# Kernel optimization log

Hardware: AMD Instinct MI355X
Metric: run time of the kernel (lower is better)

Reference implementation:

```python
import jax, jax.numpy as jnp
import numpy as np

B, N, E, L = 64, 50000, 1600000, 20
BN_EPS = 1e-5


def setup_inputs() -> dict:
    key = jax.random.key(0)
    ks = jax.random.split(key, 8)
    x = jax.random.normal(ks[0], (B, N), dtype=jnp.float32)
    edge_index = jax.random.randint(ks[1], (2, E), 0, N, dtype=jnp.int32)
    alpha = jax.random.normal(ks[2], (E,), dtype=jnp.float32)
    bias = jax.random.normal(ks[3], (E,), dtype=jnp.float32)
    # LazyLinear(num_labels) on [B, N] features
    W = jax.random.normal(ks[4], (L, N), dtype=jnp.float32) / np.sqrt(N)
    b_lin = jax.random.normal(ks[5], (L,), dtype=jnp.float32) * 0.01
    # LazyBatchNorm1d affine params over N features
    gamma = jnp.ones((N,), dtype=jnp.float32)
    beta = jnp.zeros((N,), dtype=jnp.float32)
    return {"x": x, "edge_index": edge_index, "alpha": alpha, "bias": bias,
            "W": W, "b_lin": b_lin, "gamma": gamma, "beta": beta}


def reference(x, edge_index, alpha, bias, W, b_lin, gamma, beta):
    src, dst = edge_index[0], edge_index[1]
    # gather per-edge source features and apply per-edge affine: [B, E]
    x_e = alpha * x[:, src] + bias
    # scatter-mean into destination nodes: [B, N]
    sums = jnp.zeros((x.shape[0], N), dtype=x.dtype).at[:, dst].add(x_e)
    counts = jnp.zeros((N,), dtype=x.dtype).at[dst].add(1.0)
    x_hat = sums / jnp.maximum(counts, 1.0)
    out = jnp.tanh(x_hat)
    # linear head: [B, L]
    pred = x_hat @ W.T + b_lin
    # BatchNorm1d (training mode: batch stats, biased variance)
    mu = jnp.mean(out, axis=0)
    var = jnp.var(out, axis=0)
    bn = (out - mu) / jnp.sqrt(var + BN_EPS) * gamma + beta
    return (pred, bn)
```

## Files before the change

kernel.cpp:

```cpp
#include <hip/hip_runtime.h>
#include <math.h>

#define NB 64
#define NL 20
#define BN_EPS 1e-5f

#define BIN_W 16
#define NBIN 3125
#define BIN_CAP 640
#define CHUNK 4096

#define NSB 49
#define NSBP 64
#define CAP1 36864
#define NSLICE 9

#define RB 128
#define BPR 25

__device__ __forceinline__ unsigned short f2bf(float f) {
    unsigned u = __float_as_uint(f);
    unsigned r = u + 0x7fff + ((u >> 16) & 1);
    return (unsigned short)(r >> 16);
}

__global__ __launch_bounds__(1024) void stage_kernel(
    const float* __restrict__ x, unsigned short* __restrict__ xTb,
    const int* __restrict__ src, const int* __restrict__ dst,
    const float* __restrict__ alpha, const float* __restrict__ bias,
    int* __restrict__ cnt1, uint2* __restrict__ buf1, int E, int Nn, int nA) {
    __shared__ unsigned hist[NSBP];
    __shared__ unsigned gbase[NSBP];
    __shared__ float tile[64][65];

    int tid = threadIdx.x;

    if ((int)blockIdx.x < nA) {
        int e0 = blockIdx.x * CHUNK;
        if (tid < NSBP) hist[tid] = 0;
        __syncthreads();

        uint2 pay[4];
        unsigned rk[4];
        int sb[4];
        #pragma unroll
        for (int k = 0; k < 4; ++k) {
            int e = e0 + k * 1024 + tid;
            sb[k] = -1;
            if (e < E) {
                int d = dst[e];
                int b = d >> 4;
                int dl = d & 15;
                pay[k].x = (unsigned)src[e] | ((unsigned)f2bf(alpha[e]) << 16);
                pay[k].y = (unsigned)f2bf(bias[e]) | ((unsigned)dl << 16) |
                           ((unsigned)b << 20);
                sb[k] = d >> 10;
                rk[k] = atomicAdd(&hist[sb[k]], 1u);
            }
        }
        __syncthreads();

        if (tid < NSBP) {
            unsigned v = hist[tid];
            if (v > 0) gbase[tid] = (unsigned)atomicAdd(&cnt1[tid], (int)v);
        }
        __syncthreads();

        #pragma unroll
        for (int k = 0; k < 4; ++k) {
            if (sb[k] >= 0) {
                unsigned di = gbase[sb[k]] + rk[k];
                if (di < CAP1)
                    buf1[(size_t)sb[k] * CAP1 + di] = pay[k];
            }
        }
    } else {
        int n0 = ((int)blockIdx.x - nA) * 64;
        int ln = tid & 63;
        int wv = tid >> 6;
        for (int r = wv; r < 64; r += 16) {
            int col = n0 + ln;
            tile[r][ln] = (col < Nn) ? x[r * Nn + col] : 0.f;
        }
        __syncthreads();
        for (int r = wv; r < 64; r += 16) {
            int node = n0 + r;
            if (node < Nn) xTb[(size_t)node * 64 + ln] = f2bf(tile[ln][r]);
        }
    }
}

__global__ __launch_bounds__(1024) void binB_kernel(
    const int* __restrict__ cnt1, const uint2* __restrict__ buf1,
    int* __restrict__ cursor, uint2* __restrict__ paybins) {
    __shared__ unsigned hist[64];
    __shared__ unsigned gbase[64];

    int tid = threadIdx.x;
    int sb = blockIdx.x / NSLICE;
    int slice = blockIdx.x % NSLICE;

    int lim = cnt1[sb];
    if (lim > CAP1) lim = CAP1;
    int cc = lim - slice * 4096;
    if (cc < 0) cc = 0;
    if (cc > 4096) cc = 4096;
    const uint2* pb = buf1 + (size_t)sb * CAP1 + (size_t)slice * 4096;

    if (tid < 64) hist[tid] = 0;
    __syncthreads();

    uint2 pay[4];
    unsigned rk[4];
    int lb[4];
    #pragma unroll
    for (int k = 0; k < 4; ++k) {
        int i = k * 1024 + tid;
        lb[k] = -1;
        if (i < cc) {
            pay[k] = pb[i];
            lb[k] = (int)((pay[k].y >> 20) & 63u);
            rk[k] = atomicAdd(&hist[lb[k]], 1u);
        }
    }
    __syncthreads();

    if (tid < 64) {
        unsigned v = hist[tid];
        if (v > 0)
            gbase[tid] = (unsigned)atomicAdd(&cursor[sb * 64 + tid], (int)v);
    }
    __syncthreads();

    #pragma unroll
    for (int k = 0; k < 4; ++k) {
        if (lb[k] >= 0) {
            int bin = sb * 64 + lb[k];
            unsigned di = gbase[lb[k]] + rk[k];
            if (di < BIN_CAP)
                paybins[(size_t)bin * BIN_CAP + di] = pay[k];
        }
    }
}

__global__ __launch_bounds__(256) void pull_fin5_kernel(
    const int* __restrict__ cursor, const uint2* __restrict__ paybins,
    const unsigned short* __restrict__ xTb, const float* __restrict__ W,
    const float* __restrict__ gamma, const float* __restrict__ beta,
    float* __restrict__ pred_part, float* __restrict__ bn, int Nn) {
    __shared__ __align__(16) char smem[8448];
    uint2* ed = (uint2*)smem;
    float (*xh)[66] = (float (*)[66])smem;
    float (*th)[66] = (float (*)[66])(smem + 4224);

    __shared__ float wl[NL][16];
    __shared__ unsigned h2[16], b2[16], c2[16];
    __shared__ float mu_s[16], a_s[16], be_s[16];

    const unsigned* xTbu = (const unsigned*)xTb;

    int bin = blockIdx.x;
    int tid = threadIdx.x;
    int ln = tid & 63;
    int w = tid >> 6;
    int n0 = bin * 16;
    int pair = ln >> 5;
    int h = ln & 31;

    int cnt = cursor[bin];
    if (cnt > BIN_CAP) cnt = BIN_CAP;
    const uint2* pb = paybins + (size_t)bin * BIN_CAP;

    for (int i = tid; i < NL * 16; i += 256) {
        int l = i >> 4, j = i & 15;
        wl[l][j] = W[l * Nn + n0 + j];
    }
    if (tid < 16) { h2[tid] = 0; c2[tid] = 0; }
    __syncthreads();

    uint2 pA = {0, 0}, pB = {0, 0}, pC = {0, 0};
    {
        if (tid < cnt) { pA = pb[tid]; atomicAdd(&h2[(pA.y >> 16) & 15], 1u); }
        if (tid + 256 < cnt) { pB = pb[tid + 256]; atomicAdd(&h2[(pB.y >> 16) & 15], 1u); }
        if (tid + 512 < cnt) { pC = pb[tid + 512]; atomicAdd(&h2[(pC.y >> 16) & 15], 1u); }
    }
    __syncthreads();

    if (tid < 16) {
        unsigned v = h2[tid];
        unsigned incl = v;
        #pragma unroll
        for (int off = 1; off < 16; off <<= 1) {
            unsigned t = __shfl_up(incl, off, 64);
            if (tid >= off) incl += t;
        }
        b2[tid] = incl - v;
    }
    __syncthreads();

    {
        if (tid < cnt) {
            unsigned dl = (pA.y >> 16) & 15;
            ed[b2[dl] + atomicAdd(&c2[dl], 1u)] = pA;
        }
        if (tid + 256 < cnt) {
            unsigned dl = (pB.y >> 16) & 15;
            ed[b2[dl] + atomicAdd(&c2[dl], 1u)] = pB;
        }
        if (tid + 512 < cnt) {
            unsigned dl = (pC.y >> 16) & 15;
            ed[b2[dl] + atomicAdd(&c2[dl], 1u)] = pC;
        }
    }
    __syncthreads();

    float xv_reg[4], tv_reg[4];
    #pragma unroll
    for (int k = 0; k < 4; ++k) {
        int dl = w * 4 + k;
        int node = n0 + dl;
        int n = (int)h2[dl];
        unsigned bs = b2[dl];
        float accL0 = 0.f, accH0 = 0.f, accL1 = 0.f, accH1 = 0.f;
        float bs0 = 0.f, bs1 = 0.f;
        int j = 0;
        for (; j + 3 < n; j += 4) {
            uint2 e0 = ed[bs + j + pair];
            uint2 e1 = ed[bs + j + 2 + pair];
            unsigned v0 = xTbu[(size_t)(e0.x & 0xffffu) * 32 + h];
            unsigned v1 = xTbu[(size_t)(e1.x & 0xffffu) * 32 + h];
            float al0 = __uint_as_float(e0.x & 0xffff0000u);
            float al1 = __uint_as_float(e1.x & 0xffff0000u);
            bs0 += __uint_as_float((e0.y & 0xffffu) << 16);
            bs1 += __uint_as_float((e1.y & 0xffffu) << 16);
            accL0 = fmaf(al0, __uint_as_float(v0 << 16), accL0);
            accH0 = fmaf(al0, __uint_as_float(v0 & 0xffff0000u), accH0);
            accL1 = fmaf(al1, __uint_as_float(v1 << 16), accL1);
            accH1 = fmaf(al1, __uint_as_float(v1 & 0xffff0000u), accH1);
        }
        for (; j < n; j += 2) {
            int idx = j + pair;
            bool act = idx < n;
            uint2 e0 = ed[act ? (bs + idx) : bs];
            float al0 = act ? __uint_as_float(e0.x & 0xffff0000u) : 0.f;
            float bi0 = act ? __uint_as_float((e0.y & 0xffffu) << 16) : 0.f;
            unsigned v0 = xTbu[(size_t)(e0.x & 0xffffu) * 32 + h];
            bs0 += bi0;
            accL0 = fmaf(al0, __uint_as_float(v0 << 16), accL0);
            accH0 = fmaf(al0, __uint_as_float(v0 & 0xffff0000u), accH0);
        }
        float accL = accL0 + accL1;
        float accH = accH0 + accH1;
        float bsum = bs0 + bs1;
        accL += __shfl_xor(accL, 32, 64);
        accH += __shfl_xor(accH, 32, 64);
        bsum += __shfl_xor(bsum, 32, 64);
        float inv = 1.0f / fmaxf((float)n, 1.0f);
        float xlo = (accL + bsum) * inv;
        float xhi = (accH + bsum) * inv;
        float xv = pair ? xhi : xlo;
        float tv = tanhf(xv);
        xv_reg[k] = xv;
        tv_reg[k] = tv;

        float s = tv, q = tv * tv;
        #pragma unroll
        for (int off = 32; off > 0; off >>= 1) {
            s += __shfl_xor(s, off, 64);
            q += __shfl_xor(q, off, 64);
        }
        if (ln == 0) {
            float mu = s * (1.0f / 64.0f);
            float var = fmaxf(q * (1.0f / 64.0f) - mu * mu, 0.f);
            float invs = rsqrtf(var + BN_EPS);
            mu_s[dl] = mu;
            a_s[dl] = invs * gamma[node];
            be_s[dl] = beta[node];
        }
    }
    __syncthreads();

    {
        int col = 2 * h + pair;
        #pragma unroll
        for (int k = 0; k < 4; ++k) {
            xh[w * 4 + k][col] = xv_reg[k];
            th[w * 4 + k][col] = tv_reg[k];
        }
    }
    __syncthreads();

    {
        float acc[5] = {0.f, 0.f, 0.f, 0.f, 0.f};
        #pragma unroll
        for (int n = 0; n < 16; ++n) {
            float xv = xh[n][ln];
            #pragma unroll
            for (int k = 0; k < 5; ++k)
                acc[k] = fmaf(xv, wl[w + k * 4][n], acc[k]);
        }
        #pragma unroll
        for (int k = 0; k < 5; ++k)
            pred_part[(size_t)bin * (NB * NL) + ln * NL + (w + k * 4)] = acc[k];
    }

    for (int idx = tid; idx < 16 * 64; idx += 256) {
        int noff = idx & 15, bb = idx >> 4;
        bn[bb * Nn + n0 + noff] =
            fmaf(th[noff][bb] - mu_s[noff], a_s[noff], be_s[noff]);
    }
}

__global__ __launch_bounds__(256) void reduce1_kernel(
    const float* __restrict__ part, float* __restrict__ out2, int nbin) {
    int r = blockIdx.x;
    int b0 = r * BPR;
    int b1 = b0 + BPR;
    if (b1 > nbin) b1 = nbin;
    float acc[5] = {0.f, 0.f, 0.f, 0.f, 0.f};
    for (int b = b0; b < b1; ++b) {
        const float* p = part + (size_t)b * (NB * NL);
        #pragma unroll
        for (int k = 0; k < 5; ++k)
            acc[k] += p[threadIdx.x + k * 256];
    }
    #pragma unroll
    for (int k = 0; k < 5; ++k)
        out2[(size_t)r * (NB * NL) + threadIdx.x + k * 256] = acc[k];
}

__global__ __launch_bounds__(256) void reduce2_kernel(
    const float* __restrict__ part, const float* __restrict__ b_lin,
    float* __restrict__ pred, int nblk) {
    int out = blockIdx.x * 4 + (threadIdx.x >> 6);
    if (out >= NB * NL) return;
    int ln = threadIdx.x & 63;
    float s = 0.f;
    for (int i = ln; i < nblk; i += 64)
        s += part[(size_t)i * (NB * NL) + out];
    #pragma unroll
    for (int off = 32; off > 0; off >>= 1)
        s += __shfl_xor(s, off, 64);
    if (ln == 0) pred[out] = b_lin[out % NL] + s;
}

extern "C" void kernel_launch(void* const* d_in, const int* in_sizes, int n_in,
                              void* d_out, int out_size, void* d_ws, size_t ws_size,
                              hipStream_t stream) {
    const float* x     = (const float*)d_in[0];
    const int*   ei    = (const int*)d_in[1];
    const float* alpha = (const float*)d_in[2];
    const float* bias  = (const float*)d_in[3];
    const float* W     = (const float*)d_in[4];
    const float* b_lin = (const float*)d_in[5];
    const float* gamma = (const float*)d_in[6];
    const float* beta  = (const float*)d_in[7];

    const int Nn = in_sizes[0] / NB;
    const int E  = in_sizes[1] / 2;
    const int* src = ei;
    const int* dst = ei + E;

    const int ntile = (Nn + 63) / 64;
    const int nA    = (E + CHUNK - 1) / CHUNK;

    uint2*          paybins = (uint2*)d_ws;
    uint2*          buf1    = paybins + (size_t)NBIN * BIN_CAP;
    float*          pred_part = (float*)buf1;
    char*           ubuf_end = (char*)buf1 + (size_t)NBIN * NB * NL * 4;
    unsigned short* xTb     = (unsigned short*)ubuf_end;
    int*            cnt1    = (int*)(xTb + (size_t)Nn * 64);
    int*            cursor  = cnt1 + NSBP;
    float*          out2    = (float*)(cursor + NSB * 64);

    float* pred = (float*)d_out;
    float* bn   = pred + NB * NL;

    hipMemsetAsync(cnt1, 0, (NSBP + NSB * 64) * sizeof(int), stream);

    stage_kernel<<<nA + ntile, 1024, 0, stream>>>(
        x, xTb, src, dst, alpha, bias, cnt1, buf1, E, Nn, nA);
    binB_kernel<<<NSB * NSLICE, 1024, 0, stream>>>(cnt1, buf1, cursor, paybins);
    pull_fin5_kernel<<<NBIN, 256, 0, stream>>>(cursor, paybins, xTb, W,
                                               gamma, beta, pred_part, bn, Nn);
    reduce1_kernel<<<RB, 256, 0, stream>>>(pred_part, out2, NBIN);
    reduce2_kernel<<<(NB * NL + 3) / 4, 256, 0, stream>>>(out2, b_lin, pred, RB);
}
```

Measured before the change: 183.9 us.

## Sort scatter payloads in LDS for coalesced writes; gather rows as 16B vectors

Both binning passes now prefix-scan their per-bucket histograms and stage payloads in shared memory sorted by bucket. Each bucket's global writes then come out as contiguous, coalesced runs instead of scattered stores. The pull kernel now has each lane read one 16-byte uint4 (8 bf16 batch values) per edge, with eight edges in flight per wavefront and software prefetch of the next edge. The eight partial sums are reduced with shuffles, which removes the separate register-to-LDS transpose pass and one barrier. The cost is more LDS use (32 KB sorted staging) and many more cross-lane shuffles per node.

```diff
diff --git a/kernel.cpp b/kernel.cpp
--- a/kernel.cpp
+++ b/kernel.cpp
@@ -22,6 +22,13 @@
     unsigned u = __float_as_uint(f);
     unsigned r = u + 0x7fff + ((u >> 16) & 1);
     return (unsigned short)(r >> 16);
+}
+
+__device__ __forceinline__ float bflo(unsigned u) {
+    return __uint_as_float(u << 16);
+}
+__device__ __forceinline__ float bfhi(unsigned u) {
+    return __uint_as_float(u & 0xffff0000u);
 }
 
 __global__ __launch_bounds__(1024) void stage_kernel(
@@ -31,6 +38,8 @@
     int* __restrict__ cnt1, uint2* __restrict__ buf1, int E, int Nn, int nA) {
     __shared__ unsigned hist[NSBP];
     __shared__ unsigned gbase[NSBP];
+    __shared__ unsigned sbase[NSBP];
+    __shared__ uint2 sortedA[CHUNK];
     __shared__ float tile[64][65];
 
     int tid = threadIdx.x;
@@ -62,16 +71,33 @@
 
         if (tid < NSBP) {
             unsigned v = hist[tid];
+            unsigned incl = v;
+            #pragma unroll
+            for (int off = 1; off < NSBP; off <<= 1) {
+                unsigned t = __shfl_up(incl, off, 64);
+                if (tid >= off) incl += t;
+            }
+            sbase[tid] = incl - v;
             if (v > 0) gbase[tid] = (unsigned)atomicAdd(&cnt1[tid], (int)v);
         }
         __syncthreads();
 
         #pragma unroll
+        for (int k = 0; k < 4; ++k)
+            if (sb[k] >= 0) sortedA[sbase[sb[k]] + rk[k]] = pay[k];
+        __syncthreads();
+
+        int tot = E - e0;
+        if (tot > CHUNK) tot = CHUNK;
+        #pragma unroll
         for (int k = 0; k < 4; ++k) {
-            if (sb[k] >= 0) {
-                unsigned di = gbase[sb[k]] + rk[k];
+            int i = k * 1024 + tid;
+            if (i < tot) {
+                uint2 p = sortedA[i];
+                int s2 = (int)(p.y >> 26);
+                unsigned di = gbase[s2] + (unsigned)(i - (int)sbase[s2]);
                 if (di < CAP1)
-                    buf1[(size_t)sb[k] * CAP1 + di] = pay[k];
+                    buf1[(size_t)s2 * CAP1 + di] = p;
             }
         }
     } else {
@@ -95,6 +121,8 @@
     int* __restrict__ cursor, uint2* __restrict__ paybins) {
     __shared__ unsigned hist[64];
     __shared__ unsigned gbase[64];
+    __shared__ unsigned sbase[64];
+    __shared__ uint2 sorted[4096];
 
     int tid = threadIdx.x;
     int sb = blockIdx.x / NSLICE;
@@ -127,18 +155,32 @@
 
     if (tid < 64) {
         unsigned v = hist[tid];
+        unsigned incl = v;
+        #pragma unroll
+        for (int off = 1; off < 64; off <<= 1) {
+            unsigned t = __shfl_up(incl, off, 64);
+            if (tid >= off) incl += t;
+        }
+        sbase[tid] = incl - v;
         if (v > 0)
             gbase[tid] = (unsigned)atomicAdd(&cursor[sb * 64 + tid], (int)v);
     }
     __syncthreads();
 
     #pragma unroll
+    for (int k = 0; k < 4; ++k)
+        if (lb[k] >= 0) sorted[sbase[lb[k]] + rk[k]] = pay[k];
+    __syncthreads();
+
+    #pragma unroll
     for (int k = 0; k < 4; ++k) {
-        if (lb[k] >= 0) {
-            int bin = sb * 64 + lb[k];
-            unsigned di = gbase[lb[k]] + rk[k];
+        int i = k * 1024 + tid;
+        if (i < cc) {
+            uint2 p = sorted[i];
+            int b = (int)((p.y >> 20) & 63u);
+            unsigned di = gbase[b] + (unsigned)(i - (int)sbase[b]);
             if (di < BIN_CAP)
-                paybins[(size_t)bin * BIN_CAP + di] = pay[k];
+                paybins[(size_t)(sb * 64 + b) * BIN_CAP + di] = p;
         }
     }
 }
@@ -148,24 +190,22 @@
     const unsigned short* __restrict__ xTb, const float* __restrict__ W,
     const float* __restrict__ gamma, const float* __restrict__ beta,
     float* __restrict__ pred_part, float* __restrict__ bn, int Nn) {
-    __shared__ __align__(16) char smem[8448];
-    uint2* ed = (uint2*)smem;
-    float (*xh)[66] = (float (*)[66])smem;
-    float (*th)[66] = (float (*)[66])(smem + 4224);
-
+    __shared__ __align__(16) uint2 ed[BIN_CAP];
+    __shared__ float xh[16][66];
+    __shared__ float th[16][66];
     __shared__ float wl[NL][16];
     __shared__ unsigned h2[16], b2[16], c2[16];
     __shared__ float mu_s[16], a_s[16], be_s[16];
 
-    const unsigned* xTbu = (const unsigned*)xTb;
+    const uint4* xT4 = (const uint4*)xTb;
 
     int bin = blockIdx.x;
     int tid = threadIdx.x;
     int ln = tid & 63;
     int w = tid >> 6;
     int n0 = bin * 16;
-    int pair = ln >> 5;
-    int h = ln & 31;
+    int eg = ln >> 3;
+    int q = ln & 7;
 
     int cnt = cursor[bin];
     if (cnt > BIN_CAP) cnt = BIN_CAP;
@@ -214,78 +254,88 @@
     }
     __syncthreads();
 
-    float xv_reg[4], tv_reg[4];
     #pragma unroll
     for (int k = 0; k < 4; ++k) {
         int dl = w * 4 + k;
         int node = n0 + dl;
         int n = (int)h2[dl];
         unsigned bs = b2[dl];
-        float accL0 = 0.f, accH0 = 0.f, accL1 = 0.f, accH1 = 0.f;
-        float bs0 = 0.f, bs1 = 0.f;
-        int j = 0;
-        for (; j + 3 < n; j += 4) {
-            uint2 e0 = ed[bs + j + pair];
-            uint2 e1 = ed[bs + j + 2 + pair];
-            unsigned v0 = xTbu[(size_t)(e0.x & 0xffffu) * 32 + h];
-            unsigned v1 = xTbu[(size_t)(e1.x & 0xffffu) * 32 + h];
-            float al0 = __uint_as_float(e0.x & 0xffff0000u);
-            float al1 = __uint_as_float(e1.x & 0xffff0000u);
-            bs0 += __uint_as_float((e0.y & 0xffffu) << 16);
-            bs1 += __uint_as_float((e1.y & 0xffffu) << 16);
-            accL0 = fmaf(al0, __uint_as_float(v0 << 16), accL0);
-            accH0 = fmaf(al0, __uint_as_float(v0 & 0xffff0000u), accH0);
-            accL1 = fmaf(al1, __uint_as_float(v1 << 16), accL1);
-            accH1 = fmaf(al1, __uint_as_float(v1 & 0xffff0000u), accH1);
-        }
-        for (; j < n; j += 2) {
-            int idx = j + pair;
-            bool act = idx < n;
-            uint2 e0 = ed[act ? (bs + idx) : bs];
-            float al0 = act ? __uint_as_float(e0.x & 0xffff0000u) : 0.f;
-            float bi0 = act ? __uint_as_float((e0.y & 0xffffu) << 16) : 0.f;
-            unsigned v0 = xTbu[(size_t)(e0.x & 0xffffu) * 32 + h];
-            bs0 += bi0;
-            accL0 = fmaf(al0, __uint_as_float(v0 << 16), accL0);
-            accH0 = fmaf(al0, __uint_as_float(v0 & 0xffff0000u), accH0);
-        }
-        float accL = accL0 + accL1;
-        float accH = accH0 + accH1;
-        float bsum = bs0 + bs1;
-        accL += __shfl_xor(accL, 32, 64);
-        accH += __shfl_xor(accH, 32, 64);
-        bsum += __shfl_xor(bsum, 32, 64);
+        float a0 = 0.f, a1 = 0.f, a2 = 0.f, a3 = 0.f;
+        float a4 = 0.f, a5 = 0.f, a6 = 0.f, a7 = 0.f;
+        float bsum = 0.f;
+        if (n > 0) {
+            bool act = eg < n;
+            uint2 e = ed[act ? bs + eg : bs];
+            uint4 v = xT4[(size_t)(e.x & 0xffffu) * 8 + q];
+            float al = act ? __uint_as_float(e.x & 0xffff0000u) : 0.f;
+            float bi = act ? bflo(e.y & 0xffffu) : 0.f;
+            for (int j = 8; j < n; j += 8) {
+                int idx2 = j + eg;
+                bool act2 = idx2 < n;
+                uint2 e2 = ed[act2 ? bs + idx2 : bs];
+                uint4 v2 = xT4[(size_t)(e2.x & 0xffffu) * 8 + q];
+                bsum += bi;
+                a0 = fmaf(al, bflo(v.x), a0);
+                a1 = fmaf(al, bfhi(v.x), a1);
+                a2 = fmaf(al, bflo(v.y), a2);
+                a3 = fmaf(al, bfhi(v.y), a3);
+                a4 = fmaf(al, bflo(v.z), a4);
+                a5 = fmaf(al, bfhi(v.z), a5);
+                a6 = fmaf(al, bflo(v.w), a6);
+                a7 = fmaf(al, bfhi(v.w), a7);
+                e = e2; v = v2;
+                al = act2 ? __uint_as_float(e2.x & 0xffff0000u) : 0.f;
+                bi = act2 ? bflo(e2.y & 0xffffu) : 0.f;
+            }
+            bsum += bi;
+            a0 = fmaf(al, bflo(v.x), a0);
+            a1 = fmaf(al, bfhi(v.x), a1);
+            a2 = fmaf(al, bflo(v.y), a2);
+            a3 = fmaf(al, bfhi(v.y), a3);
+            a4 = fmaf(al, bflo(v.z), a4);
+            a5 = fmaf(al, bfhi(v.z), a5);
+            a6 = fmaf(al, bflo(v.w), a6);
+            a7 = fmaf(al, bfhi(v.w), a7);
+        }
+        a0 += __shfl_xor(a0, 8, 64); a0 += __shfl_xor(a0, 16, 64); a0 += __shfl_xor(a0, 32, 64);
+        a1 += __shfl_xor(a1, 8, 64); a1 += __shfl_xor(a1, 16, 64); a1 += __shfl_xor(a1, 32, 64);
+        a2 += __shfl_xor(a2, 8, 64); a2 += __shfl_xor(a2, 16, 64); a2 += __shfl_xor(a2, 32, 64);
+        a3 += __shfl_xor(a3, 8, 64); a3 += __shfl_xor(a3, 16, 64); a3 += __shfl_xor(a3, 32, 64);
+        a4 += __shfl_xor(a4, 8, 64); a4 += __shfl_xor(a4, 16, 64); a4 += __shfl_xor(a4, 32, 64);
+        a5 += __shfl_xor(a5, 8, 64); a5 += __shfl_xor(a5, 16, 64); a5 += __shfl_xor(a5, 32, 64);
+        a6 += __shfl_xor(a6, 8, 64); a6 += __shfl_xor(a6, 16, 64); a6 += __shfl_xor(a6, 32, 64);
+        a7 += __shfl_xor(a7, 8, 64); a7 += __shfl_xor(a7, 16, 64); a7 += __shfl_xor(a7, 32, 64);
+        bsum += __shfl_xor(bsum, 8, 64); bsum += __shfl_xor(bsum, 16, 64); bsum += __shfl_xor(bsum, 32, 64);
+
+        float sel = a0;
+        sel = (eg == 1) ? a1 : sel;
+        sel = (eg == 2) ? a2 : sel;
+        sel = (eg == 3) ? a3 : sel;
+        sel = (eg == 4) ? a4 : sel;
+        sel = (eg == 5) ? a5 : sel;
+        sel = (eg == 6) ? a6 : sel;
+        sel = (eg == 7) ? a7 : sel;
+
         float inv = 1.0f / fmaxf((float)n, 1.0f);
-        float xlo = (accL + bsum) * inv;
-        float xhi = (accH + bsum) * inv;
-        float xv = pair ? xhi : xlo;
+        float xv = (sel + bsum) * inv;
         float tv = tanhf(xv);
-        xv_reg[k] = xv;
-        tv_reg[k] = tv;
-
-        float s = tv, q = tv * tv;
+        int col = 8 * q + eg;
+        xh[dl][col] = xv;
+        th[dl][col] = tv;
+
+        float s = tv, sq = tv * tv;
         #pragma unroll
         for (int off = 32; off > 0; off >>= 1) {
             s += __shfl_xor(s, off, 64);
-            q += __shfl_xor(q, off, 64);
+            sq += __shfl_xor(sq, off, 64);
         }
         if (ln == 0) {
             float mu = s * (1.0f / 64.0f);
-            float var = fmaxf(q * (1.0f / 64.0f) - mu * mu, 0.f);
+            float var = fmaxf(sq * (1.0f / 64.0f) - mu * mu, 0.f);
             float invs = rsqrtf(var + BN_EPS);
             mu_s[dl] = mu;
             a_s[dl] = invs * gamma[node];
             be_s[dl] = beta[node];
-        }
-    }
-    __syncthreads();
-
-    {
-        int col = 2 * h + pair;
-        #pragma unroll
-        for (int k = 0; k < 4; ++k) {
-            xh[w * 4 + k][col] = xv_reg[k];
-            th[w * 4 + k][col] = tv_reg[k];
         }
     }
     __syncthreads();
```

Result: faster. 176.7 us (-3.9%).
